# Kernel tuning notes

Hardware: AMD Instinct MI355X
Metric: run time of the kernel (lower is better)

The kernel has to match this reference:

```python
import jax, jax.numpy as jnp
import numpy as np

BETA = 0.9      # snn.Leaky(beta=0.9)
THRESH = 1.0    # snnTorch default threshold
SLOPE = 25.0    # surrogate.fast_sigmoid default slope
T = 16

@jax.custom_vjp
def spike_fn(x):
    return (x > 0).astype(x.dtype)

def _spike_fwd(x):
    return spike_fn(x), x

def _spike_bwd(x, g):
    # fast_sigmoid surrogate grad: 1 / (slope*|x| + 1)^2
    return (g / (SLOPE * jnp.abs(x) + 1.0) ** 2,)

spike_fn.defvjp(_spike_fwd, _spike_bwd)

def leaky_step(inp, mem):
    # snnTorch Leaky (reset_mechanism='subtract'):
    # reset based on previous membrane, then decay+integrate, then fire.
    reset = spike_fn(mem - THRESH)
    mem_new = BETA * mem + inp - reset * THRESH
    spk = spike_fn(mem_new - THRESH)
    return spk, mem_new

def setup_inputs() -> dict:
    key = jax.random.key(0)
    ks = jax.random.split(key, 7)
    B, D_IN, H, O, C = 32768, 3, 256, 25, 4
    s1 = 1.0 / np.sqrt(D_IN)
    s2 = 1.0 / np.sqrt(H)
    return {
        "x": jax.random.normal(ks[0], (B, D_IN), jnp.float32),
        "W1": jax.random.uniform(ks[1], (D_IN, H), jnp.float32, -s1, s1),
        "b1": jax.random.uniform(ks[2], (H,), jnp.float32, -s1, s1),
        "W2": jax.random.uniform(ks[3], (H, H), jnp.float32, -s2, s2),
        "b2": jax.random.uniform(ks[4], (H,), jnp.float32, -s2, s2),
        "Wout": jax.random.uniform(ks[5], (O, H, C), jnp.float32, -s2, s2),
        "bout": jax.random.uniform(ks[6], (O, C), jnp.float32, -s2, s2),
    }

def reference(x, W1, b1, W2, b2, Wout, bout):
    B = x.shape[0]
    O, H, C = Wout.shape
    # fc1 input current is identical every timestep (x is static)
    cur1 = x @ W1 + b1  # [B,H]
    mem1 = jnp.zeros((B, H), x.dtype)
    mem2 = jnp.zeros((B, H), x.dtype)
    memo = jnp.zeros((B, O, C), x.dtype)
    counts = jnp.zeros((B, O, C), x.dtype)

    def step(carry, _):
        mem1, mem2, memo, counts = carry
        spk1, mem1 = leaky_step(cur1, mem1)
        spk2, mem2 = leaky_step(spk1 @ W2 + b2, mem2)
        curo = jnp.einsum('bh,ohc->boc', spk2, Wout) + bout  # 25 heads batched
        spko, memo = leaky_step(curo, memo)
        return (mem1, mem2, memo, counts + spko), None

    (mem1, mem2, memo, counts), _ = jax.lax.scan(
        step, (mem1, mem2, memo, counts), None, length=T)
    # equivalent to list of 25 spike-count tensors [B,4]; stacked as [B,25,4]
    return counts
```

## Files before the change

### kernel.cpp

```cpp
#include <hip/hip_runtime.h>
#include <stdint.h>

#define TT 16

typedef float v2f __attribute__((ext_vector_type(2)));

__device__ __forceinline__ float lstep(float mem, float cur) {
    const float reset = (mem > 1.0f) ? 1.0f : 0.0f;
    return __builtin_fmaf(0.9f, mem, cur) - reset;
}

__device__ __forceinline__ uint64_t mask_pair(uint32_t p, int tp) {
    const uint32_t lo = ((p >> (2 * tp)) & 1u) * 0x3F800000u;
    const uint32_t hi = ((p >> (2 * tp + 1)) & 1u) * 0x3F800000u;
    return ((uint64_t)hi << 32) | (uint64_t)lo;
}

#define PKFMA_BLO(acc, mp, w)                                              \
    asm("v_pk_fma_f32 %0, %1, %2, %0 op_sel:[0,0,0] op_sel_hi:[1,0,1]"     \
        : "+v"(acc) : "s"(mp), "v"(w))
#define PKFMA_BHI(acc, mp, w)                                              \
    asm("v_pk_fma_f32 %0, %1, %2, %0 op_sel:[0,1,0] op_sel_hi:[1,1,1]"     \
        : "+v"(acc) : "s"(mp), "v"(w))

__global__ __launch_bounds__(256, 4) void snn_fast(
    const float* __restrict__ x,
    const float* __restrict__ W1,
    const float* __restrict__ b1,
    const float* __restrict__ W2,
    const float* __restrict__ b2,
    const float* __restrict__ Wout,
    const float* __restrict__ bout,
    float* __restrict__ out)
{
#pragma clang fp contract(off)
    const int tid = threadIdx.x;
    const int l   = tid & 63;
    const int b   = blockIdx.x * 4 + (tid >> 6);

    const float x0 = x[b * 3 + 0], x1 = x[b * 3 + 1], x2 = x[b * 3 + 2];
    const float4 w1r0 = ((const float4*)W1)[l];
    const float4 w1r1 = ((const float4*)W1)[64 + l];
    const float4 w1r2 = ((const float4*)W1)[128 + l];
    const float4 b1v  = ((const float4*)b1)[l];

    const float wa0[4] = {w1r0.x, w1r0.y, w1r0.z, w1r0.w};
    const float wa1[4] = {w1r1.x, w1r1.y, w1r1.z, w1r1.w};
    const float wa2[4] = {w1r2.x, w1r2.y, w1r2.z, w1r2.w};
    const float bb1[4] = {b1v.x, b1v.y, b1v.z, b1v.w};

    uint32_t b1r[4];
#pragma unroll
    for (int i = 0; i < 4; ++i) {
        const float cur = fmaf(x2, wa2[i], fmaf(x1, wa1[i], x0 * wa0[i])) + bb1[i];
        float mem = 0.f; uint32_t p = 0;
#pragma unroll
        for (int t = 0; t < TT; ++t) {
            mem = lstep(mem, cur);
            if (mem > 1.0f) p |= (1u << t);
        }
        b1r[i] = p;
    }

    v2f accB[4][8];
#pragma unroll
    for (int jj = 0; jj < 4; ++jj)
#pragma unroll
        for (int tp = 0; tp < 8; ++tp) accB[jj][tp] = (v2f)0.f;

    const float4* W2v = (const float4*)W2;
    for (int h4 = 0; h4 < 64; ++h4) {
#pragma unroll
        for (int c = 0; c < 4; ++c) {
            const uint32_t p =
                (uint32_t)__builtin_amdgcn_readlane((int)b1r[c], h4);
            if (p) {
                const float4 w = W2v[(h4 * 4 + c) * 64 + l];
                const v2f w01 = {w.x, w.y};
                const v2f w23 = {w.z, w.w};
#pragma unroll
                for (int tp = 0; tp < 8; ++tp) {
                    const uint64_t mp = mask_pair(p, tp);
                    PKFMA_BLO(accB[0][tp], mp, w01);
                    PKFMA_BHI(accB[1][tp], mp, w01);
                    PKFMA_BLO(accB[2][tp], mp, w23);
                    PKFMA_BHI(accB[3][tp], mp, w23);
                }
            }
        }
    }

    const float4 b2v = ((const float4*)b2)[l];
    const float b2a[4] = {b2v.x, b2v.y, b2v.z, b2v.w};
    uint32_t b2r[4];
#pragma unroll
    for (int i = 0; i < 4; ++i) {
        float mem = 0.f; uint32_t p = 0;
#pragma unroll
        for (int t = 0; t < TT; ++t) {
            const float a = (t & 1) ? accB[i][t >> 1].y : accB[i][t >> 1].x;
            const float cur = a + b2a[i];
            mem = lstep(mem, cur);
            if (mem > 1.0f) p |= (1u << t);
        }
        b2r[i] = p;
    }

    const int oc1 = l;
    const int oc2 = (l < 50) ? (l + 50) : 99;
    const int base1 = (oc1 >> 2) * 1024 + (oc1 & 3);
    const int base2 = (oc2 >> 2) * 1024 + (oc2 & 3);

    v2f accC[2][8];
#pragma unroll
    for (int o = 0; o < 2; ++o)
#pragma unroll
        for (int tp = 0; tp < 8; ++tp) accC[o][tp] = (v2f)0.f;

    for (int h4 = 0; h4 < 64; ++h4) {
#pragma unroll
        for (int c = 0; c < 4; ++c) {
            const uint32_t p =
                (uint32_t)__builtin_amdgcn_readlane((int)b2r[c], h4);
            if (p) {
                const int h = h4 * 4 + c;
                const v2f w = {Wout[base1 + h * 4], Wout[base2 + h * 4]};
#pragma unroll
                for (int tp = 0; tp < 8; ++tp) {
                    const uint64_t mp = mask_pair(p, tp);
                    PKFMA_BLO(accC[0][tp], mp, w);
                    PKFMA_BHI(accC[1][tp], mp, w);
                }
            }
        }
    }

    const float bo1 = bout[oc1], bo2 = bout[oc2];
    float memA = 0.f, memB = 0.f;
    int cntA = 0, cntB = 0;
#pragma unroll
    for (int t = 0; t < TT; ++t) {
        const float aA = (t & 1) ? accC[0][t >> 1].y : accC[0][t >> 1].x;
        const float aB = (t & 1) ? accC[1][t >> 1].y : accC[1][t >> 1].x;
        const float curA = aA + bo1;
        const float curB = aB + bo2;
        memA = lstep(memA, curA);
        memB = lstep(memB, curB);
        if (memA > 1.0f) ++cntA;
        if (memB > 1.0f) ++cntB;
    }
    if (l < 50) {
        out[b * 100 + oc1] = (float)cntA;
        out[b * 100 + oc2] = (float)cntB;
    }
}

extern "C" void kernel_launch(void* const* d_in, const int* in_sizes, int n_in,
                              void* d_out, int out_size, void* d_ws, size_t ws_size,
                              hipStream_t stream) {
    const float* x    = (const float*)d_in[0];
    const float* W1   = (const float*)d_in[1];
    const float* b1   = (const float*)d_in[2];
    const float* W2   = (const float*)d_in[3];
    const float* b2   = (const float*)d_in[4];
    const float* Wout = (const float*)d_in[5];
    const float* bout = (const float*)d_in[6];
    float* out = (float*)d_out;

    const int B = in_sizes[0] / 3;
    snn_fast<<<B / 4, 256, 0, stream>>>(x, W1, b1, W2, b2, Wout, bout, out);
}
```

Before: 689.2 us.

## Process two batch samples per wavefront to reuse weight loads

Each wavefront now handles two batch rows instead of one, so every W2 and Wout weight load feeds two sets of accumulators. Accumulator registers double (64 to 128 floats for layer 2), and launch bounds drop from 4 to 2 blocks per CU so the extra registers fit. Because a row is skipped only when neither sample has a spike, the spike-sparsity skip becomes less effective. Lower occupancy may also hide load latency less well.

```diff
diff --git a/kernel.cpp b/kernel.cpp
--- a/kernel.cpp
+++ b/kernel.cpp
@@ -23,7 +23,7 @@
     asm("v_pk_fma_f32 %0, %1, %2, %0 op_sel:[0,1,0] op_sel_hi:[1,1,1]"     \
         : "+v"(acc) : "s"(mp), "v"(w))
 
-__global__ __launch_bounds__(256, 4) void snn_fast(
+__global__ __launch_bounds__(256, 2) void snn_fast(
     const float* __restrict__ x,
     const float* __restrict__ W1,
     const float* __restrict__ b1,
@@ -36,9 +36,9 @@
 #pragma clang fp contract(off)
     const int tid = threadIdx.x;
     const int l   = tid & 63;
-    const int b   = blockIdx.x * 4 + (tid >> 6);
-
-    const float x0 = x[b * 3 + 0], x1 = x[b * 3 + 1], x2 = x[b * 3 + 2];
+    const int b0  = blockIdx.x * 8 + (tid >> 6);
+    const int b1s = b0 + 4;
+
     const float4 w1r0 = ((const float4*)W1)[l];
     const float4 w1r1 = ((const float4*)W1)[64 + l];
     const float4 w1r2 = ((const float4*)W1)[128 + l];
@@ -49,42 +49,59 @@
     const float wa2[4] = {w1r2.x, w1r2.y, w1r2.z, w1r2.w};
     const float bb1[4] = {b1v.x, b1v.y, b1v.z, b1v.w};
 
-    uint32_t b1r[4];
-#pragma unroll
-    for (int i = 0; i < 4; ++i) {
-        const float cur = fmaf(x2, wa2[i], fmaf(x1, wa1[i], x0 * wa0[i])) + bb1[i];
-        float mem = 0.f; uint32_t p = 0;
-#pragma unroll
-        for (int t = 0; t < TT; ++t) {
-            mem = lstep(mem, cur);
-            if (mem > 1.0f) p |= (1u << t);
-        }
-        b1r[i] = p;
-    }
-
-    v2f accB[4][8];
-#pragma unroll
-    for (int jj = 0; jj < 4; ++jj)
-#pragma unroll
-        for (int tp = 0; tp < 8; ++tp) accB[jj][tp] = (v2f)0.f;
+    const float xs[2][3] = {
+        {x[b0 * 3 + 0], x[b0 * 3 + 1], x[b0 * 3 + 2]},
+        {x[b1s * 3 + 0], x[b1s * 3 + 1], x[b1s * 3 + 2]}};
+
+    uint32_t bits1[2][4];
+#pragma unroll
+    for (int s = 0; s < 2; ++s) {
+#pragma unroll
+        for (int i = 0; i < 4; ++i) {
+            const float cur = fmaf(xs[s][2], wa2[i],
+                             fmaf(xs[s][1], wa1[i], xs[s][0] * wa0[i])) + bb1[i];
+            float mem = 0.f; uint32_t p = 0;
+#pragma unroll
+            for (int t = 0; t < TT; ++t) {
+                mem = lstep(mem, cur);
+                if (mem > 1.0f) p |= (1u << t);
+            }
+            bits1[s][i] = p;
+        }
+    }
+
+    v2f aB[2][4][8];
+#pragma unroll
+    for (int s = 0; s < 2; ++s)
+#pragma unroll
+        for (int jj = 0; jj < 4; ++jj)
+#pragma unroll
+            for (int tp = 0; tp < 8; ++tp) aB[s][jj][tp] = (v2f)0.f;
 
     const float4* W2v = (const float4*)W2;
     for (int h4 = 0; h4 < 64; ++h4) {
 #pragma unroll
         for (int c = 0; c < 4; ++c) {
-            const uint32_t p =
-                (uint32_t)__builtin_amdgcn_readlane((int)b1r[c], h4);
-            if (p) {
+            const uint32_t p0 =
+                (uint32_t)__builtin_amdgcn_readlane((int)bits1[0][c], h4);
+            const uint32_t p1 =
+                (uint32_t)__builtin_amdgcn_readlane((int)bits1[1][c], h4);
+            if (p0 | p1) {
                 const float4 w = W2v[(h4 * 4 + c) * 64 + l];
                 const v2f w01 = {w.x, w.y};
                 const v2f w23 = {w.z, w.w};
 #pragma unroll
                 for (int tp = 0; tp < 8; ++tp) {
-                    const uint64_t mp = mask_pair(p, tp);
-                    PKFMA_BLO(accB[0][tp], mp, w01);
-                    PKFMA_BHI(accB[1][tp], mp, w01);
-                    PKFMA_BLO(accB[2][tp], mp, w23);
-                    PKFMA_BHI(accB[3][tp], mp, w23);
+                    const uint64_t mp0 = mask_pair(p0, tp);
+                    const uint64_t mp1 = mask_pair(p1, tp);
+                    PKFMA_BLO(aB[0][0][tp], mp0, w01);
+                    PKFMA_BHI(aB[0][1][tp], mp0, w01);
+                    PKFMA_BLO(aB[0][2][tp], mp0, w23);
+                    PKFMA_BHI(aB[0][3][tp], mp0, w23);
+                    PKFMA_BLO(aB[1][0][tp], mp1, w01);
+                    PKFMA_BHI(aB[1][1][tp], mp1, w01);
+                    PKFMA_BLO(aB[1][2][tp], mp1, w23);
+                    PKFMA_BHI(aB[1][3][tp], mp1, w23);
                 }
             }
         }
@@ -92,18 +109,21 @@
 
     const float4 b2v = ((const float4*)b2)[l];
     const float b2a[4] = {b2v.x, b2v.y, b2v.z, b2v.w};
-    uint32_t b2r[4];
-#pragma unroll
-    for (int i = 0; i < 4; ++i) {
-        float mem = 0.f; uint32_t p = 0;
-#pragma unroll
-        for (int t = 0; t < TT; ++t) {
-            const float a = (t & 1) ? accB[i][t >> 1].y : accB[i][t >> 1].x;
-            const float cur = a + b2a[i];
-            mem = lstep(mem, cur);
-            if (mem > 1.0f) p |= (1u << t);
-        }
-        b2r[i] = p;
+    uint32_t bits2[2][4];
+#pragma unroll
+    for (int s = 0; s < 2; ++s) {
+#pragma unroll
+        for (int i = 0; i < 4; ++i) {
+            float mem = 0.f; uint32_t p = 0;
+#pragma unroll
+            for (int t = 0; t < TT; ++t) {
+                const float a = (t & 1) ? aB[s][i][t >> 1].y : aB[s][i][t >> 1].x;
+                const float cur = a + b2a[i];
+                mem = lstep(mem, cur);
+                if (mem > 1.0f) p |= (1u << t);
+            }
+            bits2[s][i] = p;
+        }
     }
 
     const int oc1 = l;
@@ -111,47 +131,57 @@
     const int base1 = (oc1 >> 2) * 1024 + (oc1 & 3);
     const int base2 = (oc2 >> 2) * 1024 + (oc2 & 3);
 
-    v2f accC[2][8];
-#pragma unroll
-    for (int o = 0; o < 2; ++o)
-#pragma unroll
-        for (int tp = 0; tp < 8; ++tp) accC[o][tp] = (v2f)0.f;
+    v2f aC[2][2][8];
+#pragma unroll
+    for (int s = 0; s < 2; ++s)
+#pragma unroll
+        for (int o = 0; o < 2; ++o)
+#pragma unroll
+            for (int tp = 0; tp < 8; ++tp) aC[s][o][tp] = (v2f)0.f;
 
     for (int h4 = 0; h4 < 64; ++h4) {
 #pragma unroll
         for (int c = 0; c < 4; ++c) {
-            const uint32_t p =
-                (uint32_t)__builtin_amdgcn_readlane((int)b2r[c], h4);
-            if (p) {
+            const uint32_t p0 =
+                (uint32_t)__builtin_amdgcn_readlane((int)bits2[0][c], h4);
+            const uint32_t p1 =
+                (uint32_t)__builtin_amdgcn_readlane((int)bits2[1][c], h4);
+            if (p0 | p1) {
                 const int h = h4 * 4 + c;
                 const v2f w = {Wout[base1 + h * 4], Wout[base2 + h * 4]};
 #pragma unroll
                 for (int tp = 0; tp < 8; ++tp) {
-                    const uint64_t mp = mask_pair(p, tp);
-                    PKFMA_BLO(accC[0][tp], mp, w);
-                    PKFMA_BHI(accC[1][tp], mp, w);
+                    const uint64_t mp0 = mask_pair(p0, tp);
+                    const uint64_t mp1 = mask_pair(p1, tp);
+                    PKFMA_BLO(aC[0][0][tp], mp0, w);
+                    PKFMA_BHI(aC[0][1][tp], mp0, w);
+                    PKFMA_BLO(aC[1][0][tp], mp1, w);
+                    PKFMA_BHI(aC[1][1][tp], mp1, w);
                 }
             }
         }
     }
 
     const float bo1 = bout[oc1], bo2 = bout[oc2];
-    float memA = 0.f, memB = 0.f;
-    int cntA = 0, cntB = 0;
-#pragma unroll
-    for (int t = 0; t < TT; ++t) {
-        const float aA = (t & 1) ? accC[0][t >> 1].y : accC[0][t >> 1].x;
-        const float aB = (t & 1) ? accC[1][t >> 1].y : accC[1][t >> 1].x;
-        const float curA = aA + bo1;
-        const float curB = aB + bo2;
-        memA = lstep(memA, curA);
-        memB = lstep(memB, curB);
-        if (memA > 1.0f) ++cntA;
-        if (memB > 1.0f) ++cntB;
+    int cnt[2][2] = {{0, 0}, {0, 0}};
+#pragma unroll
+    for (int s = 0; s < 2; ++s) {
+        float memA = 0.f, memB = 0.f;
+#pragma unroll
+        for (int t = 0; t < TT; ++t) {
+            const float aA = (t & 1) ? aC[s][0][t >> 1].y : aC[s][0][t >> 1].x;
+            const float aB2 = (t & 1) ? aC[s][1][t >> 1].y : aC[s][1][t >> 1].x;
+            memA = lstep(memA, aA + bo1);
+            memB = lstep(memB, aB2 + bo2);
+            if (memA > 1.0f) ++cnt[s][0];
+            if (memB > 1.0f) ++cnt[s][1];
+        }
     }
     if (l < 50) {
-        out[b * 100 + oc1] = (float)cntA;
-        out[b * 100 + oc2] = (float)cntB;
+        out[b0 * 100 + oc1]  = (float)cnt[0][0];
+        out[b0 * 100 + oc2]  = (float)cnt[0][1];
+        out[b1s * 100 + oc1] = (float)cnt[1][0];
+        out[b1s * 100 + oc2] = (float)cnt[1][1];
     }
 }
 
@@ -168,5 +198,5 @@
     float* out = (float*)d_out;
 
     const int B = in_sizes[0] / 3;
-    snn_fast<<<B / 4, 256, 0, stream>>>(x, W1, b1, W2, b2, Wout, bout, out);
-}
+    snn_fast<<<B / 8, 256, 0, stream>>>(x, W1, b1, W2, b2, Wout, bout, out);
+}
```

New measurement: 1.126 ms. +63.4%, slower.

## Stage Wout in LDS per block with two-pass load and 512-thread blocks

Applied to the files above, without the earlier changes.

Doubles the block to 8 wavefronts (8 batch rows) and cooperatively stages Wout into shared memory in two 128-hidden halves, transposed to [h][100] layout. Each wave then reads its output weights from LDS instead of issuing strided scalar global loads. This targets the latency of the scattered global Wout reads in the output layer. In exchange it adds block-wide barriers, a 51 KB LDS footprint that limits occupancy, and redundant staging work in every block.

```diff
diff --git a/kernel.cpp b/kernel.cpp
--- a/kernel.cpp
+++ b/kernel.cpp
@@ -23,7 +23,7 @@
     asm("v_pk_fma_f32 %0, %1, %2, %0 op_sel:[0,1,0] op_sel_hi:[1,1,1]"     \
         : "+v"(acc) : "s"(mp), "v"(w))
 
-__global__ __launch_bounds__(256, 4) void snn_fast(
+__global__ __launch_bounds__(512, 2) void snn_fast(
     const float* __restrict__ x,
     const float* __restrict__ W1,
     const float* __restrict__ b1,
@@ -36,7 +36,9 @@
 #pragma clang fp contract(off)
     const int tid = threadIdx.x;
     const int l   = tid & 63;
-    const int b   = blockIdx.x * 4 + (tid >> 6);
+    const int b   = blockIdx.x * 8 + (tid >> 6);
+
+    __shared__ float wlds[128 * 100];
 
     const float x0 = x[b * 3 + 0], x1 = x[b * 3 + 1], x2 = x[b * 3 + 2];
     const float4 w1r0 = ((const float4*)W1)[l];
@@ -108,28 +110,36 @@
 
     const int oc1 = l;
     const int oc2 = (l < 50) ? (l + 50) : 99;
-    const int base1 = (oc1 >> 2) * 1024 + (oc1 & 3);
-    const int base2 = (oc2 >> 2) * 1024 + (oc2 & 3);
 
-    v2f accC[2][8];
+    v2f aC[2][8];
 #pragma unroll
     for (int o = 0; o < 2; ++o)
 #pragma unroll
-        for (int tp = 0; tp < 8; ++tp) accC[o][tp] = (v2f)0.f;
+        for (int tp = 0; tp < 8; ++tp) aC[o][tp] = (v2f)0.f;
 
-    for (int h4 = 0; h4 < 64; ++h4) {
+    for (int pass = 0; pass < 2; ++pass) {
+        const int h0 = pass * 128;
+        __syncthreads();
+        for (int hb = 0; hb < 25; ++hb) {
+            wlds[(tid >> 2) * 100 + hb * 4 + (tid & 3)] =
+                Wout[hb * 1024 + h0 * 4 + tid];
+        }
+        __syncthreads();
+
+        for (int h4 = 0; h4 < 32; ++h4) {
 #pragma unroll
-        for (int c = 0; c < 4; ++c) {
-            const uint32_t p =
-                (uint32_t)__builtin_amdgcn_readlane((int)b2r[c], h4);
-            if (p) {
-                const int h = h4 * 4 + c;
-                const v2f w = {Wout[base1 + h * 4], Wout[base2 + h * 4]};
+            for (int c = 0; c < 4; ++c) {
+                const uint32_t p = (uint32_t)__builtin_amdgcn_readlane(
+                    (int)b2r[c], pass * 32 + h4);
+                if (p) {
+                    const int hl = h4 * 4 + c;
+                    const v2f w = {wlds[hl * 100 + oc1], wlds[hl * 100 + oc2]};
 #pragma unroll
-                for (int tp = 0; tp < 8; ++tp) {
-                    const uint64_t mp = mask_pair(p, tp);
-                    PKFMA_BLO(accC[0][tp], mp, w);
-                    PKFMA_BHI(accC[1][tp], mp, w);
+                    for (int tp = 0; tp < 8; ++tp) {
+                        const uint64_t mp = mask_pair(p, tp);
+                        PKFMA_BLO(aC[0][tp], mp, w);
+                        PKFMA_BHI(aC[1][tp], mp, w);
+                    }
                 }
             }
         }
@@ -140,12 +150,10 @@
     int cntA = 0, cntB = 0;
 #pragma unroll
     for (int t = 0; t < TT; ++t) {
-        const float aA = (t & 1) ? accC[0][t >> 1].y : accC[0][t >> 1].x;
-        const float aB = (t & 1) ? accC[1][t >> 1].y : accC[1][t >> 1].x;
-        const float curA = aA + bo1;
-        const float curB = aB + bo2;
-        memA = lstep(memA, curA);
-        memB = lstep(memB, curB);
+        const float aA = (t & 1) ? aC[0][t >> 1].y : aC[0][t >> 1].x;
+        const float aB = (t & 1) ? aC[1][t >> 1].y : aC[1][t >> 1].x;
+        memA = lstep(memA, aA + bo1);
+        memB = lstep(memB, aB + bo2);
         if (memA > 1.0f) ++cntA;
         if (memB > 1.0f) ++cntB;
     }
@@ -168,5 +176,5 @@
     float* out = (float*)d_out;
 
     const int B = in_sizes[0] / 3;
-    snn_fast<<<B / 4, 256, 0, stream>>>(x, W1, b1, W2, b2, Wout, bout, out);
+    snn_fast<<<B / 8, 512, 0, stream>>>(x, W1, b1, W2, b2, Wout, bout, out);
 }
```

Measured after the change: 706.1 us. 1.02x slower.
